# Kernel tuning notes

Measured on AMD Instinct MI355X. Metric: run time of the kernel, lower is better.

The kernel has to match this reference:

```python
import jax, jax.numpy as jnp
import numpy as np

EPS = 1e-5
N, K, CIN, COUT = 100000, 27, 64, 128


def sparse_conv(x, nbr, W):
    # x: [N, C]; nbr: [N, K] with sentinel index N meaning 'no neighbor'
    x_pad = jnp.concatenate([x, jnp.zeros((1, x.shape[1]), x.dtype)], axis=0)  # [N+1, C]
    g = x_pad[nbr]  # gather: [N, K, C]
    return jnp.einsum('nkc,kcd->nd', g, W)  # per-offset GEMM, scatter to output sites


def bn_relu(y, gamma, beta):
    # BatchNorm over active sites (training-mode batch statistics), then ReLU
    mu = y.mean(axis=0)
    var = y.var(axis=0)
    return jax.nn.relu((y - mu) * jax.lax.rsqrt(var + EPS) * gamma + beta)


def setup_inputs() -> dict:
    key = jax.random.key(0)
    ks = jax.random.split(key, 5)
    x = jax.random.normal(ks[0], (N, CIN), dtype=jnp.float32)
    # sentinel N indicates missing neighbor (maps to zero-padded row)
    nbr = jax.random.randint(ks[1], (N, K), 0, N + 1)
    W1 = jax.random.normal(ks[2], (K, CIN, COUT), dtype=jnp.float32) * (1.0 / np.sqrt(K * CIN))
    W2 = jax.random.normal(ks[3], (K, COUT, COUT), dtype=jnp.float32) * (1.0 / np.sqrt(K * COUT))
    W_skip = jax.random.normal(ks[4], (CIN, COUT), dtype=jnp.float32) * (1.0 / np.sqrt(CIN))
    return {
        'x': x, 'nbr': nbr,
        'W1': W1, 'gamma1': jnp.ones((COUT,), jnp.float32), 'beta1': jnp.zeros((COUT,), jnp.float32),
        'W2': W2, 'gamma2': jnp.ones((COUT,), jnp.float32), 'beta2': jnp.zeros((COUT,), jnp.float32),
        'W_skip': W_skip,
    }


def reference(x, nbr, W1, gamma1, beta1, W2, gamma2, beta2, W_skip):
    identity = x @ W_skip                      # 1x1 conv skip (same coords)
    h = bn_relu(sparse_conv(x, nbr, W1), gamma1, beta1)
    h = bn_relu(sparse_conv(h, nbr, W2), gamma2, beta2)
    return h + identity
```

## Files before the change

### kernel.cpp

```cpp
#include <hip/hip_runtime.h>
#include <hip/hip_bf16.h>

#define NSITES 100000
#define KOFFS 27
#define CIN 64
#define COUT 128

typedef unsigned short u16;
typedef __attribute__((ext_vector_type(8))) short s16x8;
typedef __attribute__((ext_vector_type(4))) float f32x4;

static __device__ __forceinline__ u16 f2bf(float f) {
    union { float f; unsigned u; } x; x.f = f;
    return (u16)((x.u + 0x7FFFu + ((x.u >> 16) & 1u)) >> 16);
}
static __device__ __forceinline__ float bf2f(u16 v) {
    union { unsigned u; float f; } x; x.u = ((unsigned)v) << 16;
    return x.f;
}

__global__ void prep_kernel(const float* __restrict__ W1, const float* __restrict__ W2,
                            const float* __restrict__ Wsk,
                            u16* __restrict__ W1t, u16* __restrict__ W2t,
                            u16* __restrict__ Wskt, float* __restrict__ zero_area) {
    int i = blockIdx.x * 256 + threadIdx.x;
    if (i < 27 * 64 * 128) {
        int k = i / 8192, r = i & 8191, d = r >> 6, c = r & 63;
        W1t[i] = f2bf(W1[k * 8192 + c * 128 + d]);
        return;
    }
    i -= 27 * 64 * 128;
    if (i < 27 * 128 * 128) {
        int k = i / 16384, r = i & 16383, d = r >> 7, c = r & 127;
        W2t[i] = f2bf(W2[k * 16384 + c * 128 + d]);
        return;
    }
    i -= 27 * 128 * 128;
    if (i < 8192) {
        int d = i >> 6, c = i & 63;
        Wskt[i] = f2bf(Wsk[c * 128 + d]);
        return;
    }
    i -= 8192;
    zero_area[i] = 0.0f;
}

__global__ void convert_x_kernel(const float* __restrict__ x, u16* __restrict__ xb) {
    long long e = ((long long)blockIdx.x * 256 + threadIdx.x) * 8;
    if (e >= (long long)(NSITES + 1) * CIN) return;
    s16x8 o;
    if (e < (long long)NSITES * CIN) {
        float4 v0 = *(const float4*)(x + e);
        float4 v1 = *(const float4*)(x + e + 4);
        o[0] = (short)f2bf(v0.x); o[1] = (short)f2bf(v0.y);
        o[2] = (short)f2bf(v0.z); o[3] = (short)f2bf(v0.w);
        o[4] = (short)f2bf(v1.x); o[5] = (short)f2bf(v1.y);
        o[6] = (short)f2bf(v1.z); o[7] = (short)f2bf(v1.w);
    } else {
#pragma unroll
        for (int j = 0; j < 8; ++j) o[j] = 0;
    }
    *(s16x8*)(xb + e) = o;
}

template <int CK, bool IDENT_FUSE, bool STATS>
__global__ __launch_bounds__(256, 4) void conv_kernel(
    const u16* __restrict__ xin, const int* __restrict__ nbr,
    const u16* __restrict__ Wt, u16* __restrict__ yout,
    float* __restrict__ psum, float* __restrict__ psq, int nk,
    const u16* __restrict__ Wskt, float* __restrict__ outid) {
    constexpr int KSTEPS = CK / 32;
    constexpr int CPR = CK / 8;
    constexpr int SWZ = CPR - 1;
    constexpr int RPP = 256 / CPR;
    constexpr int NPASS = 64 / RPP;
    __shared__ __align__(16) u16 a_tile[2][64 * CK];

    const int tid = threadIdx.x;
    const int wave = tid >> 6;
    const int lane = tid & 63;
    const int m = lane & 15;
    const int q = lane >> 4;
    const int n0 = blockIdx.x * 64;
    const int wc = wave * 32;
    const int srow = tid / CPR;
    const int schunk = tid % CPR;

    f32x4 acc[4][2];
#pragma unroll
    for (int rt = 0; rt < 4; ++rt)
#pragma unroll
        for (int ct = 0; ct < 2; ++ct)
#pragma unroll
            for (int r = 0; r < 4; ++r) acc[rt][ct][r] = 0.0f;

    int nidx[NPASS];
    s16x8 ag[NPASS];
#pragma unroll
    for (int p = 0; p < NPASS; ++p) {
        int row = n0 + p * RPP + srow;
        nidx[p] = (row < NSITES) ? nbr[row * KOFFS] : NSITES;
    }
#pragma unroll
    for (int p = 0; p < NPASS; ++p)
        ag[p] = *(const s16x8*)(xin + (long long)nidx[p] * CK + schunk * 8);
#pragma unroll
    for (int p = 0; p < NPASS; ++p) {
        int row = n0 + p * RPP + srow;
        nidx[p] = (row < NSITES && nk > 1) ? nbr[row * KOFFS + 1] : NSITES;
    }
#pragma unroll
    for (int p = 0; p < NPASS; ++p) {
        int r = p * RPP + srow;
        *(s16x8*)(a_tile[0] + r * CK + ((schunk ^ (r & SWZ)) * 8)) = ag[p];
    }
    __syncthreads();

    for (int k = 0; k < nk; ++k) {
        const u16* abuf = a_tile[k & 1];
        u16* wbuf = a_tile[(k + 1) & 1];
        const bool more = (k + 1 < nk);

        s16x8 bf[2][KSTEPS];
        const u16* wb = Wt + (long long)k * (COUT * CK);
#pragma unroll
        for (int ct = 0; ct < 2; ++ct)
#pragma unroll
            for (int ks = 0; ks < KSTEPS; ++ks)
                bf[ct][ks] = *(const s16x8*)(wb + (wc + ct * 16 + m) * CK + ks * 32 + q * 8);

        if (more) {
#pragma unroll
            for (int p = 0; p < NPASS; ++p)
                ag[p] = *(const s16x8*)(xin + (long long)nidx[p] * CK + schunk * 8);
#pragma unroll
            for (int p = 0; p < NPASS; ++p) {
                int row = n0 + p * RPP + srow;
                nidx[p] = (row < NSITES && k + 2 < nk) ? nbr[row * KOFFS + k + 2] : NSITES;
            }
        }

#pragma unroll
        for (int ks = 0; ks < KSTEPS; ++ks) {
            s16x8 af[4];
#pragma unroll
            for (int rt = 0; rt < 4; ++rt) {
                int r = rt * 16 + m;
                af[rt] = *(const s16x8*)(abuf + r * CK + (((ks * 4 + q) ^ (r & SWZ)) * 8));
            }
#pragma unroll
            for (int rt = 0; rt < 4; ++rt)
#pragma unroll
                for (int ct = 0; ct < 2; ++ct)
                    acc[rt][ct] = __builtin_amdgcn_mfma_f32_16x16x32_bf16(
                        af[rt], bf[ct][ks], acc[rt][ct], 0, 0, 0);
        }

        if (more) {
#pragma unroll
            for (int p = 0; p < NPASS; ++p) {
                int r = p * RPP + srow;
                *(s16x8*)(wbuf + r * CK + ((schunk ^ (r & SWZ)) * 8)) = ag[p];
            }
        }
        __syncthreads();
    }

#pragma unroll
    for (int rt = 0; rt < 4; ++rt) {
        int rowb = n0 + rt * 16 + q * 4;
#pragma unroll
        for (int ct = 0; ct < 2; ++ct) {
            int col = wc + ct * 16 + m;
#pragma unroll
            for (int r = 0; r < 4; ++r) {
                int row = rowb + r;
                if (row < NSITES) yout[(long long)row * COUT + col] = f2bf(acc[rt][ct][r]);
            }
        }
    }

    if (STATS) {
#pragma unroll
        for (int ct = 0; ct < 2; ++ct) {
            float s = 0.f, ss = 0.f;
#pragma unroll
            for (int rt = 0; rt < 4; ++rt)
#pragma unroll
                for (int r = 0; r < 4; ++r) {
                    float v = acc[rt][ct][r];
                    s += v; ss += v * v;
                }
            s += __shfl_xor(s, 16); ss += __shfl_xor(ss, 16);
            s += __shfl_xor(s, 32); ss += __shfl_xor(ss, 32);
            if (q == 0) {
                int col = wc + ct * 16 + m;
                int slot = blockIdx.x & 63;
                atomicAdd(psum + slot * COUT + col, s);
                atomicAdd(psq + slot * COUT + col, ss);
            }
        }
    }

    if (IDENT_FUSE) {
#pragma unroll
        for (int rt = 0; rt < 4; ++rt)
#pragma unroll
            for (int ct = 0; ct < 2; ++ct)
#pragma unroll
                for (int r = 0; r < 4; ++r) acc[rt][ct][r] = 0.0f;
        s16x8 aid[NPASS];
#pragma unroll
        for (int p = 0; p < NPASS; ++p) {
            int row = n0 + p * RPP + srow;
            long long idx = (row < NSITES) ? row : NSITES;
            aid[p] = *(const s16x8*)(xin + idx * CK + schunk * 8);
        }
        s16x8 bfi[2][KSTEPS];
#pragma unroll
        for (int ct = 0; ct < 2; ++ct)
#pragma unroll
            for (int ks = 0; ks < KSTEPS; ++ks)
                bfi[ct][ks] = *(const s16x8*)(Wskt + (wc + ct * 16 + m) * CK + ks * 32 + q * 8);
#pragma unroll
        for (int p = 0; p < NPASS; ++p) {
            int r = p * RPP + srow;
            *(s16x8*)(a_tile[0] + r * CK + ((schunk ^ (r & SWZ)) * 8)) = aid[p];
        }
        __syncthreads();
#pragma unroll
        for (int ks = 0; ks < KSTEPS; ++ks) {
            s16x8 af[4];
#pragma unroll
            for (int rt = 0; rt < 4; ++rt) {
                int r = rt * 16 + m;
                af[rt] = *(const s16x8*)(a_tile[0] + r * CK + (((ks * 4 + q) ^ (r & SWZ)) * 8));
            }
#pragma unroll
            for (int rt = 0; rt < 4; ++rt)
#pragma unroll
                for (int ct = 0; ct < 2; ++ct)
                    acc[rt][ct] = __builtin_amdgcn_mfma_f32_16x16x32_bf16(
                        af[rt], bfi[ct][ks], acc[rt][ct], 0, 0, 0);
        }
#pragma unroll
        for (int rt = 0; rt < 4; ++rt) {
            int rowb = n0 + rt * 16 + q * 4;
#pragma unroll
            for (int ct = 0; ct < 2; ++ct) {
                int col = wc + ct * 16 + m;
#pragma unroll
                for (int r = 0; r < 4; ++r) {
                    int row = rowb + r;
                    if (row < NSITES) outid[(long long)row * COUT + col] = acc[rt][ct][r];
                }
            }
        }
    }
}

__global__ void bn_stats_kernel(const float* __restrict__ psum, const float* __restrict__ psq,
                                const float* __restrict__ gamma, const float* __restrict__ beta,
                                float* __restrict__ ab) {
    int col = threadIdx.x;
    float s = 0.f, ss = 0.f;
    for (int i = 0; i < 64; ++i) { s += psum[i * COUT + col]; ss += psq[i * COUT + col]; }
    const float inv_n = 1.0f / (float)NSITES;
    float mu = s * inv_n;
    float var = ss * inv_n - mu * mu;
    float rs = rsqrtf(var + 1e-5f);
    float a = gamma[col] * rs;
    ab[col] = a;
    ab[COUT + col] = beta[col] - mu * a;
}

__global__ void bn_apply_kernel(const u16* __restrict__ y, const float* __restrict__ ab,
                                u16* __restrict__ h) {
    long long e = ((long long)blockIdx.x * 256 + threadIdx.x) * 8;
    if (e >= (long long)(NSITES + 1) * COUT) return;
    s16x8 o;
    if (e < (long long)NSITES * COUT) {
        int cb = (int)(e & (COUT - 1));
        s16x8 v = *(const s16x8*)(y + e);
#pragma unroll
        for (int j = 0; j < 8; ++j) {
            float r = bf2f((u16)v[j]) * ab[cb + j] + ab[COUT + cb + j];
            o[j] = (short)f2bf(fmaxf(r, 0.f));
        }
    } else {
#pragma unroll
        for (int j = 0; j < 8; ++j) o[j] = 0;
    }
    *(s16x8*)(h + e) = o;
}

__global__ void final_kernel(const u16* __restrict__ y, const float* __restrict__ ab,
                             float* __restrict__ out) {
    long long e = ((long long)blockIdx.x * 256 + threadIdx.x) * 8;
    if (e >= (long long)NSITES * COUT) return;
    int cb = (int)(e & (COUT - 1));
    s16x8 v = *(const s16x8*)(y + e);
    float4 i0 = *(const float4*)(out + e);
    float4 i1 = *(const float4*)(out + e + 4);
    float is[8] = {i0.x, i0.y, i0.z, i0.w, i1.x, i1.y, i1.z, i1.w};
    float os[8];
#pragma unroll
    for (int j = 0; j < 8; ++j) {
        float r = bf2f((u16)v[j]) * ab[cb + j] + ab[COUT + cb + j];
        os[j] = fmaxf(r, 0.f) + is[j];
    }
    *(float4*)(out + e) = make_float4(os[0], os[1], os[2], os[3]);
    *(float4*)(out + e + 4) = make_float4(os[4], os[5], os[6], os[7]);
}

extern "C" void kernel_launch(void* const* d_in, const int* in_sizes, int n_in,
                              void* d_out, int out_size, void* d_ws, size_t ws_size,
                              hipStream_t stream) {
    const float* x   = (const float*)d_in[0];
    const int*   nbr = (const int*)d_in[1];
    const float* W1  = (const float*)d_in[2];
    const float* g1  = (const float*)d_in[3];
    const float* b1  = (const float*)d_in[4];
    const float* W2  = (const float*)d_in[5];
    const float* g2  = (const float*)d_in[6];
    const float* b2  = (const float*)d_in[7];
    const float* Wsk = (const float*)d_in[8];
    float* out = (float*)d_out;

    char* ws = (char*)d_ws;
    u16*   xb   = (u16*)(ws);
    u16*   W1t  = (u16*)(ws + 12800128);
    u16*   W2t  = (u16*)(ws + 13242496);
    u16*   Wskt = (u16*)(ws + 14127232);
    u16*   y    = (u16*)(ws + 14143616);
    u16*   h1   = (u16*)(ws + 39743616);
    float* ps1  = (float*)(ws + 65343872);
    float* pq1  = ps1 + 8192;
    float* ps2  = pq1 + 8192;
    float* pq2  = ps2 + 8192;
    float* ab1  = pq2 + 8192;
    float* ab2  = ab1 + 256;

    const int NBLK = (NSITES + 63) / 64;

    prep_kernel<<<2752, 256, 0, stream>>>(W1, W2, Wsk, W1t, W2t, Wskt, ps1);
    convert_x_kernel<<<3126, 256, 0, stream>>>(x, xb);
    conv_kernel<64, true, true><<<NBLK, 256, 0, stream>>>(xb, nbr, W1t, y, ps1, pq1, KOFFS, Wskt, out);
    bn_stats_kernel<<<1, 128, 0, stream>>>(ps1, pq1, g1, b1, ab1);
    bn_apply_kernel<<<6251, 256, 0, stream>>>(y, ab1, h1);
    conv_kernel<128, false, true><<<NBLK, 256, 0, stream>>>(h1, nbr, W2t, y, ps2, pq2, KOFFS, nullptr, nullptr);
    bn_stats_kernel<<<1, 128, 0, stream>>>(ps2, pq2, g2, b2, ab2);
    final_kernel<<<6250, 256, 0, stream>>>(y, ab2, out);
}
```

Measured before the change: 467.2 us.

## Shard second sparse conv by channel groups into L2-sized planes with partial-sum reduction

The second convolution is split into 8 channel-group shards. Each shard stores its 16-channel slice of h as a compact plane, so the random neighbor gathers hit a smaller working set that fits better in cache. Each shard writes bf16 partial outputs, and a reduce kernel sums them, writes y and accumulates the BN statistics. Work is split into two halves of sites to bound the partial buffer. The change also raises occupancy on conv1 and uses nontemporal stores. The cost is extra partial-sum traffic, bf16 rounding of the partials, and several more launches. The path only runs if the workspace is large enough.

```diff
diff --git a/kernel.cpp b/kernel.cpp
--- a/kernel.cpp
+++ b/kernel.cpp
@@ -5,6 +5,8 @@
 #define KOFFS 27
 #define CIN 64
 #define COUT 128
+#define NHALF 50048
+#define PSTRIDE ((NSITES + 2) * 16)
 
 typedef unsigned short u16;
 typedef __attribute__((ext_vector_type(8))) short s16x8;
@@ -20,29 +22,39 @@
 }
 
 __global__ void prep_kernel(const float* __restrict__ W1, const float* __restrict__ W2,
-                            const float* __restrict__ Wsk,
-                            u16* __restrict__ W1t, u16* __restrict__ W2t,
+                            const float* __restrict__ Wsk, u16* __restrict__ W1t,
+                            u16* __restrict__ W2t, u16* __restrict__ W2p,
                             u16* __restrict__ Wskt, float* __restrict__ zero_area) {
     int i = blockIdx.x * 256 + threadIdx.x;
-    if (i < 27 * 64 * 128) {
+    if (i < 221184) {
         int k = i / 8192, r = i & 8191, d = r >> 6, c = r & 63;
         W1t[i] = f2bf(W1[k * 8192 + c * 128 + d]);
         return;
     }
-    i -= 27 * 64 * 128;
-    if (i < 27 * 128 * 128) {
+    i -= 221184;
+    if (i < 442368) {
         int k = i / 16384, r = i & 16383, d = r >> 7, c = r & 127;
         W2t[i] = f2bf(W2[k * 16384 + c * 128 + d]);
         return;
     }
-    i -= 27 * 128 * 128;
+    i -= 442368;
+    if (i < 458752) {
+        int j = i & 31, t = i >> 5;
+        int d = t & 127; t >>= 7;
+        int s = t % 14, g = t / 14;
+        int k = 2 * s + (j >> 4);
+        int c = 16 * g + (j & 15);
+        W2p[i] = (k < 27) ? f2bf(W2[k * 16384 + c * 128 + d]) : (u16)0;
+        return;
+    }
+    i -= 458752;
     if (i < 8192) {
         int d = i >> 6, c = i & 63;
         Wskt[i] = f2bf(Wsk[c * 128 + d]);
         return;
     }
     i -= 8192;
-    zero_area[i] = 0.0f;
+    if (i < 32768) zero_area[i] = 0.0f;
 }
 
 __global__ void convert_x_kernel(const float* __restrict__ x, u16* __restrict__ xb) {
@@ -63,8 +75,15 @@
     *(s16x8*)(xb + e) = o;
 }
 
-template <int CK, bool IDENT_FUSE, bool STATS>
-__global__ __launch_bounds__(256, 4) void conv_kernel(
+__global__ void pack_nbr_kernel(const int* __restrict__ nbr, int* __restrict__ nbr28) {
+    int i = blockIdx.x * 256 + threadIdx.x;
+    if (i >= NSITES * 28) return;
+    int n = i / 28, k = i - n * 28;
+    nbr28[i] = (k < 27) ? nbr[n * KOFFS + k] : NSITES;
+}
+
+template <int CK, bool IDENT_FUSE, bool STATS, int OCC>
+__global__ __launch_bounds__(256, OCC) void conv_kernel(
     const u16* __restrict__ xin, const int* __restrict__ nbr,
     const u16* __restrict__ Wt, u16* __restrict__ yout,
     float* __restrict__ psum, float* __restrict__ psq, int nk,
@@ -175,7 +194,9 @@
 #pragma unroll
             for (int r = 0; r < 4; ++r) {
                 int row = rowb + r;
-                if (row < NSITES) yout[(long long)row * COUT + col] = f2bf(acc[rt][ct][r]);
+                if (row < NSITES)
+                    __builtin_nontemporal_store((u16)f2bf(acc[rt][ct][r]),
+                                                yout + (long long)row * COUT + col);
             }
         }
     }
@@ -256,6 +277,144 @@
                 }
             }
         }
+    }
+}
+
+__global__ __launch_bounds__(256, 6) void conv2_sharded_kernel(
+    const u16* __restrict__ hp, const int* __restrict__ nbr28,
+    const u16* __restrict__ W2p, u16* __restrict__ pp, int half_base) {
+    __shared__ __align__(16) u16 a_tile[2][64 * 32];
+
+    const int bid = blockIdx.x;
+    const int g = bid & 7;
+    const int tile = bid >> 3;
+    const u16* plane = hp + (long long)g * PSTRIDE;
+    const u16* wbase = W2p + g * (14 * 128 * 32);
+
+    const int tid = threadIdx.x;
+    const int lane = tid & 63;
+    const int wave = tid >> 6;
+    const int m = lane & 15;
+    const int q = lane >> 4;
+    const int wc = wave * 32;
+    const int n0 = half_base + tile * 64;
+    const int r = tid >> 2;
+    const int p = tid & 3;
+    const int ko_off = p >> 1, hsel = p & 1;
+    const int myrow = n0 + r;
+    const bool rv = myrow < NSITES;
+    const int* nb = nbr28 + (long long)myrow * 28;
+
+    int nidx14[14];
+#pragma unroll
+    for (int s = 0; s < 14; ++s) nidx14[s] = rv ? nb[2 * s + ko_off] : NSITES;
+
+    f32x4 acc[4][2];
+#pragma unroll
+    for (int rt = 0; rt < 4; ++rt)
+#pragma unroll
+        for (int ct = 0; ct < 2; ++ct)
+#pragma unroll
+            for (int rr = 0; rr < 4; ++rr) acc[rt][ct][rr] = 0.0f;
+
+    {
+        s16x8 ag = *(const s16x8*)(plane + (long long)nidx14[0] * 16 + hsel * 8);
+        *(s16x8*)(&a_tile[0][r * 32 + ((p ^ (r & 3)) * 8)]) = ag;
+    }
+    __syncthreads();
+
+#pragma unroll
+    for (int s = 0; s < 14; ++s) {
+        const u16* abuf = a_tile[s & 1];
+        u16* wbuf = a_tile[(s + 1) & 1];
+
+        s16x8 bf0 = *(const s16x8*)(wbase + ((s * 128 + wc + m) * 32) + q * 8);
+        s16x8 bf1 = *(const s16x8*)(wbase + ((s * 128 + wc + 16 + m) * 32) + q * 8);
+
+        s16x8 agn;
+        if (s + 1 < 14)
+            agn = *(const s16x8*)(plane + (long long)nidx14[s + 1] * 16 + hsel * 8);
+
+        s16x8 af[4];
+#pragma unroll
+        for (int rt = 0; rt < 4; ++rt) {
+            int rr = rt * 16 + m;
+            af[rt] = *(const s16x8*)(abuf + rr * 32 + ((q ^ (rr & 3)) * 8));
+        }
+#pragma unroll
+        for (int rt = 0; rt < 4; ++rt) {
+            acc[rt][0] = __builtin_amdgcn_mfma_f32_16x16x32_bf16(af[rt], bf0, acc[rt][0], 0, 0, 0);
+            acc[rt][1] = __builtin_amdgcn_mfma_f32_16x16x32_bf16(af[rt], bf1, acc[rt][1], 0, 0, 0);
+        }
+
+        if (s + 1 < 14)
+            *(s16x8*)(wbuf + r * 32 + ((p ^ (r & 3)) * 8)) = agn;
+        __syncthreads();
+    }
+
+    u16* ppg = pp + ((long long)g * NHALF + (tile * 64)) * 128;
+#pragma unroll
+    for (int rt = 0; rt < 4; ++rt) {
+        int rowb = rt * 16 + q * 4;
+#pragma unroll
+        for (int ct = 0; ct < 2; ++ct) {
+            int col = wc + ct * 16 + m;
+#pragma unroll
+            for (int rr = 0; rr < 4; ++rr) {
+                int row_l = rowb + rr;
+                if (n0 + row_l < NSITES)
+                    __builtin_nontemporal_store((u16)f2bf(acc[rt][ct][rr]),
+                                                ppg + (long long)row_l * 128 + col);
+            }
+        }
+    }
+}
+
+__global__ void reduce2_kernel(const u16* __restrict__ pp, u16* __restrict__ y,
+                               float* __restrict__ psum, float* __restrict__ psq,
+                               int half_base, int nsites_half) {
+    __shared__ float cs[128], cq[128];
+    const int tid = threadIdx.x;
+    if (tid < 128) { cs[tid] = 0.f; cq[tid] = 0.f; }
+    __syncthreads();
+
+    const int sl = blockIdx.x * 16 + (tid >> 4);
+    const int ch0 = (tid & 15) * 8;
+    float v[8];
+#pragma unroll
+    for (int j = 0; j < 8; ++j) v[j] = 0.f;
+    if (sl < nsites_half) {
+#pragma unroll
+        for (int g = 0; g < 8; ++g) {
+            s16x8 t = *(const s16x8*)(pp + ((long long)g * NHALF + sl) * 128 + ch0);
+#pragma unroll
+            for (int j = 0; j < 8; ++j) v[j] += bf2f((u16)t[j]);
+        }
+        s16x8 o;
+#pragma unroll
+        for (int j = 0; j < 8; ++j) o[j] = (short)f2bf(v[j]);
+        *(s16x8*)(y + ((long long)(half_base + sl)) * 128 + ch0) = o;
+    }
+    float s[8], ss[8];
+#pragma unroll
+    for (int j = 0; j < 8; ++j) { s[j] = v[j]; ss[j] = v[j] * v[j]; }
+#pragma unroll
+    for (int j = 0; j < 8; ++j) {
+        s[j] += __shfl_xor(s[j], 16); ss[j] += __shfl_xor(ss[j], 16);
+        s[j] += __shfl_xor(s[j], 32); ss[j] += __shfl_xor(ss[j], 32);
+    }
+    if ((tid & 63) < 16) {
+#pragma unroll
+        for (int j = 0; j < 8; ++j) {
+            atomicAdd(&cs[ch0 + j], s[j]);
+            atomicAdd(&cq[ch0 + j], ss[j]);
+        }
+    }
+    __syncthreads();
+    if (tid < 128) {
+        int slot = blockIdx.x & 63;
+        atomicAdd(psum + slot * COUT + tid, cs[tid]);
+        atomicAdd(psq + slot * COUT + tid, cq[tid]);
     }
 }
 
@@ -274,6 +433,31 @@
     ab[COUT + col] = beta[col] - mu * a;
 }
 
+__global__ void bn_apply_sharded_kernel(const u16* __restrict__ y, const float* __restrict__ ab,
+                                        u16* __restrict__ hp) {
+    int i = blockIdx.x * 256 + threadIdx.x;
+    if (i >= 8 * (NSITES + 1) * 2) return;
+    int g = i / ((NSITES + 1) * 2);
+    int rem = i - g * ((NSITES + 1) * 2);
+    int r = rem >> 1, half = rem & 1;
+    int ch0 = 16 * g + 8 * half;
+    s16x8 o;
+    if (r < NSITES) {
+        s16x8 v = *(const s16x8*)(y + (long long)r * 128 + ch0);
+#pragma unroll
+        for (int j = 0; j < 8; ++j) {
+            float t = bf2f((u16)v[j]) * ab[ch0 + j] + ab[COUT + ch0 + j];
+            o[j] = (short)f2bf(fmaxf(t, 0.f));
+        }
+    } else {
+#pragma unroll
+        for (int j = 0; j < 8; ++j) o[j] = 0;
+    }
+    u16* dst = hp + (long long)g * PSTRIDE + (long long)r * 16 + half * 8;
+#pragma unroll
+    for (int j = 0; j < 8; ++j) __builtin_nontemporal_store((u16)o[j], dst + j);
+}
+
 __global__ void bn_apply_kernel(const u16* __restrict__ y, const float* __restrict__ ab,
                                 u16* __restrict__ h) {
     long long e = ((long long)blockIdx.x * 256 + threadIdx.x) * 8;
@@ -328,27 +512,44 @@
     float* out = (float*)d_out;
 
     char* ws = (char*)d_ws;
-    u16*   xb   = (u16*)(ws);
-    u16*   W1t  = (u16*)(ws + 12800128);
-    u16*   W2t  = (u16*)(ws + 13242496);
-    u16*   Wskt = (u16*)(ws + 14127232);
-    u16*   y    = (u16*)(ws + 14143616);
-    u16*   h1   = (u16*)(ws + 39743616);
-    float* ps1  = (float*)(ws + 65343872);
-    float* pq1  = ps1 + 8192;
-    float* ps2  = pq1 + 8192;
-    float* pq2  = ps2 + 8192;
-    float* ab1  = pq2 + 8192;
-    float* ab2  = ab1 + 256;
+    u16*   xb    = (u16*)(ws);
+    u16*   W1t   = (u16*)(ws + 12800128);
+    u16*   W2t   = (u16*)(ws + 13242496);
+    u16*   Wskt  = (u16*)(ws + 14127232);
+    u16*   y     = (u16*)(ws + 14143616);
+    u16*   h1    = (u16*)(ws + 39743616);
+    float* ps1   = (float*)(ws + 65343872);
+    float* pq1   = ps1 + 8192;
+    float* ps2   = pq1 + 8192;
+    float* pq2   = ps2 + 8192;
+    float* ab1   = pq2 + 8192;
+    float* ab2   = ab1 + 256;
+    u16*   W2p   = (u16*)(ws + 65476992);
+    int*   nbr28 = (int*)(ws + 66394496);
+    u16*   hp    = (u16*)(ws + 77594496);
+    u16*   pp    = (u16*)(ws + 103195008);
+    const size_t WS_NEED = 205693312ULL;
 
     const int NBLK = (NSITES + 63) / 64;
-
-    prep_kernel<<<2752, 256, 0, stream>>>(W1, W2, Wsk, W1t, W2t, Wskt, ps1);
+    const bool sharded = (ws_size >= WS_NEED);
+
+    prep_kernel<<<4544, 256, 0, stream>>>(W1, W2, Wsk, W1t, W2t, W2p, Wskt, ps1);
     convert_x_kernel<<<3126, 256, 0, stream>>>(x, xb);
-    conv_kernel<64, true, true><<<NBLK, 256, 0, stream>>>(xb, nbr, W1t, y, ps1, pq1, KOFFS, Wskt, out);
+    conv_kernel<64, true, true, 6><<<NBLK, 256, 0, stream>>>(xb, nbr, W1t, y, ps1, pq1, KOFFS, Wskt, out);
     bn_stats_kernel<<<1, 128, 0, stream>>>(ps1, pq1, g1, b1, ab1);
-    bn_apply_kernel<<<6251, 256, 0, stream>>>(y, ab1, h1);
-    conv_kernel<128, false, true><<<NBLK, 256, 0, stream>>>(h1, nbr, W2t, y, ps2, pq2, KOFFS, nullptr, nullptr);
+
+    if (sharded) {
+        pack_nbr_kernel<<<(NSITES * 28 + 255) / 256, 256, 0, stream>>>(nbr, nbr28);
+        bn_apply_sharded_kernel<<<(8 * (NSITES + 1) * 2 + 255) / 256, 256, 0, stream>>>(y, ab1, hp);
+        conv2_sharded_kernel<<<8 * 782, 256, 0, stream>>>(hp, nbr28, W2p, pp, 0);
+        reduce2_kernel<<<3128, 256, 0, stream>>>(pp, y, ps2, pq2, 0, 50048);
+        conv2_sharded_kernel<<<8 * 781, 256, 0, stream>>>(hp, nbr28, W2p, pp, NHALF);
+        reduce2_kernel<<<3122, 256, 0, stream>>>(pp, y, ps2, pq2, NHALF, NSITES - NHALF);
+    } else {
+        bn_apply_kernel<<<6251, 256, 0, stream>>>(y, ab1, h1);
+        conv_kernel<128, false, true, 4><<<NBLK, 256, 0, stream>>>(h1, nbr, W2t, y, ps2, pq2, KOFFS,
+                                                                   nullptr, nullptr);
+    }
     bn_stats_kernel<<<1, 128, 0, stream>>>(ps2, pq2, g2, b2, ab2);
     final_kernel<<<6250, 256, 0, stream>>>(y, ab2, out);
 }
```

After: 620.2 us. 1.33x slower.

## Deepen gather prefetch pipeline to two offsets ahead with lighter barriers

Applied to the files above, without the earlier changes.

The conv kernel now gathers neighbor rows two kernel offsets ahead in two register sets, and loads neighbor indices four offsets ahead. The loop is unrolled by two through a lambda that swaps the register buffers. __syncthreads is replaced by an inline-asm LDS wait plus s_barrier, and the second conv drops its launch bound occupancy from 4 to 3 to make room for the extra registers. The aim is to hide global gather latency better, at the cost of more registers and lower occupancy. The prep kernel also gains a bounds guard on zeroing.

```diff
diff --git a/kernel.cpp b/kernel.cpp
--- a/kernel.cpp
+++ b/kernel.cpp
@@ -17,6 +17,10 @@
 static __device__ __forceinline__ float bf2f(u16 v) {
     union { unsigned u; float f; } x; x.u = ((unsigned)v) << 16;
     return x.f;
+}
+
+static __device__ __forceinline__ void lds_barrier() {
+    __asm__ __volatile__("s_waitcnt lgkmcnt(0)\n\ts_barrier" ::: "memory");
 }
 
 __global__ void prep_kernel(const float* __restrict__ W1, const float* __restrict__ W2,
@@ -42,7 +46,7 @@
         return;
     }
     i -= 8192;
-    zero_area[i] = 0.0f;
+    if (i < 32768) zero_area[i] = 0.0f;
 }
 
 __global__ void convert_x_kernel(const float* __restrict__ x, u16* __restrict__ xb) {
@@ -63,8 +67,8 @@
     *(s16x8*)(xb + e) = o;
 }
 
-template <int CK, bool IDENT_FUSE, bool STATS>
-__global__ __launch_bounds__(256, 4) void conv_kernel(
+template <int CK, bool IDENT_FUSE, bool STATS, int OCC>
+__global__ __launch_bounds__(256, OCC) void conv_kernel(
     const u16* __restrict__ xin, const int* __restrict__ nbr,
     const u16* __restrict__ Wt, u16* __restrict__ yout,
     float* __restrict__ psum, float* __restrict__ psq, int nk,
@@ -94,33 +98,39 @@
 #pragma unroll
             for (int r = 0; r < 4; ++r) acc[rt][ct][r] = 0.0f;
 
-    int nidx[NPASS];
-    s16x8 ag[NPASS];
+    int nidx0[NPASS], nidx1[NPASS], tmp[NPASS];
+    s16x8 ag0[NPASS], ag1[NPASS];
 #pragma unroll
     for (int p = 0; p < NPASS; ++p) {
         int row = n0 + p * RPP + srow;
-        nidx[p] = (row < NSITES) ? nbr[row * KOFFS] : NSITES;
+        tmp[p] = (row < NSITES) ? nbr[row * KOFFS] : NSITES;
     }
 #pragma unroll
     for (int p = 0; p < NPASS; ++p)
-        ag[p] = *(const s16x8*)(xin + (long long)nidx[p] * CK + schunk * 8);
+        ag0[p] = *(const s16x8*)(xin + (long long)tmp[p] * CK + schunk * 8);
 #pragma unroll
     for (int p = 0; p < NPASS; ++p) {
         int row = n0 + p * RPP + srow;
-        nidx[p] = (row < NSITES && nk > 1) ? nbr[row * KOFFS + 1] : NSITES;
+        tmp[p] = (row < NSITES && nk > 1) ? nbr[row * KOFFS + 1] : NSITES;
+    }
+#pragma unroll
+    for (int p = 0; p < NPASS; ++p)
+        ag1[p] = *(const s16x8*)(xin + (long long)tmp[p] * CK + schunk * 8);
+#pragma unroll
+    for (int p = 0; p < NPASS; ++p) {
+        int row = n0 + p * RPP + srow;
+        nidx0[p] = (row < NSITES && nk > 2) ? nbr[row * KOFFS + 2] : NSITES;
+        nidx1[p] = (row < NSITES && nk > 3) ? nbr[row * KOFFS + 3] : NSITES;
     }
 #pragma unroll
     for (int p = 0; p < NPASS; ++p) {
         int r = p * RPP + srow;
-        *(s16x8*)(a_tile[0] + r * CK + ((schunk ^ (r & SWZ)) * 8)) = ag[p];
+        *(s16x8*)(a_tile[0] + r * CK + ((schunk ^ (r & SWZ)) * 8)) = ag0[p];
     }
     __syncthreads();
 
-    for (int k = 0; k < nk; ++k) {
-        const u16* abuf = a_tile[k & 1];
-        u16* wbuf = a_tile[(k + 1) & 1];
-        const bool more = (k + 1 < nk);
-
+    auto stage = [&](int k, s16x8 (&g_in)[NPASS], int (&idx_in)[NPASS],
+                     s16x8 (&g_out)[NPASS], const u16* abuf, u16* wbuf) {
         s16x8 bf[2][KSTEPS];
         const u16* wb = Wt + (long long)k * (COUT * CK);
 #pragma unroll
@@ -129,15 +139,15 @@
             for (int ks = 0; ks < KSTEPS; ++ks)
                 bf[ct][ks] = *(const s16x8*)(wb + (wc + ct * 16 + m) * CK + ks * 32 + q * 8);
 
-        if (more) {
+        if (k + 2 < nk) {
 #pragma unroll
             for (int p = 0; p < NPASS; ++p)
-                ag[p] = *(const s16x8*)(xin + (long long)nidx[p] * CK + schunk * 8);
-#pragma unroll
-            for (int p = 0; p < NPASS; ++p) {
-                int row = n0 + p * RPP + srow;
-                nidx[p] = (row < NSITES && k + 2 < nk) ? nbr[row * KOFFS + k + 2] : NSITES;
-            }
+                g_in[p] = *(const s16x8*)(xin + (long long)idx_in[p] * CK + schunk * 8);
+        }
+#pragma unroll
+        for (int p = 0; p < NPASS; ++p) {
+            int row = n0 + p * RPP + srow;
+            idx_in[p] = (row < NSITES && k + 4 < nk) ? nbr[row * KOFFS + k + 4] : NSITES;
         }
 
 #pragma unroll
@@ -156,14 +166,19 @@
                         af[rt], bf[ct][ks], acc[rt][ct], 0, 0, 0);
         }
 
-        if (more) {
+        if (k + 1 < nk) {
 #pragma unroll
             for (int p = 0; p < NPASS; ++p) {
                 int r = p * RPP + srow;
-                *(s16x8*)(wbuf + r * CK + ((schunk ^ (r & SWZ)) * 8)) = ag[p];
-            }
-        }
-        __syncthreads();
+                *(s16x8*)(wbuf + r * CK + ((schunk ^ (r & SWZ)) * 8)) = g_out[p];
+            }
+        }
+        lds_barrier();
+    };
+
+    for (int k = 0; k < nk; k += 2) {
+        stage(k, ag0, nidx0, ag1, a_tile[0], a_tile[1]);
+        if (k + 1 < nk) stage(k + 1, ag1, nidx1, ag0, a_tile[1], a_tile[0]);
     }
 
 #pragma unroll
@@ -345,10 +360,11 @@
 
     prep_kernel<<<2752, 256, 0, stream>>>(W1, W2, Wsk, W1t, W2t, Wskt, ps1);
     convert_x_kernel<<<3126, 256, 0, stream>>>(x, xb);
-    conv_kernel<64, true, true><<<NBLK, 256, 0, stream>>>(xb, nbr, W1t, y, ps1, pq1, KOFFS, Wskt, out);
+    conv_kernel<64, true, true, 4><<<NBLK, 256, 0, stream>>>(xb, nbr, W1t, y, ps1, pq1, KOFFS, Wskt, out);
     bn_stats_kernel<<<1, 128, 0, stream>>>(ps1, pq1, g1, b1, ab1);
     bn_apply_kernel<<<6251, 256, 0, stream>>>(y, ab1, h1);
-    conv_kernel<128, false, true><<<NBLK, 256, 0, stream>>>(h1, nbr, W2t, y, ps2, pq2, KOFFS, nullptr, nullptr);
+    conv_kernel<128, false, true, 3><<<NBLK, 256, 0, stream>>>(h1, nbr, W2t, y, ps2, pq2, KOFFS,
+                                                               nullptr, nullptr);
     bn_stats_kernel<<<1, 128, 0, stream>>>(ps2, pq2, g2, b2, ab2);
     final_kernel<<<6250, 256, 0, stream>>>(y, ab2, out);
 }
```

Result: slower. 482.3 us (+3.2%).
